# Performance work log

Measured on AMD Instinct MI355X. Metric: run time of the kernel, lower is better.

Reference implementation:

```python
import jax, jax.numpy as jnp
import numpy as np

HEIGHT = 1024.0
WIDTH = 1024.0
OUTER_BOUND_WEIGHT = 0.01


def setup_inputs() -> dict:
    key = jax.random.key(0)
    k1, k2 = jax.random.split(key)
    B, K = 4096, 4096
    # predictions roughly in-image scale
    output = jax.random.normal(k1, (B, K, 2), dtype=jnp.float32) * 300.0 + 512.0
    target = jax.random.uniform(k2, (B, K, 2), dtype=jnp.float32) * 1224.0 - 100.0
    return {"output": output, "target": target}


def reference(output, target):
    # output, target: [B, K, 2]
    B = target.shape[0]
    tx = target[..., 0]
    ty = target[..., 1]
    oob = (tx < 0) | (tx > WIDTH) | (ty < 0) | (ty > HEIGHT)  # [B, K]
    weight = jnp.where(oob, OUTER_BOUND_WEIGHT, 1.0).astype(output.dtype)
    sq = jnp.sum((output - target) ** 2, axis=-1)  # [B, K] per-keypoint MSE
    raw_batch_loss = jnp.sum(weight * sq)
    return raw_batch_loss / B
```

## Files before the change

kernel.cpp:

```cpp
#include <hip/hip_runtime.h>


#define WIDTH_F  1024.0f
#define HEIGHT_F 1024.0f
#define OOB_W    0.01f

__device__ __forceinline__ float kp_pair(float4 o, float4 t) {
    float dx = o.x - t.x;
    float dy = o.y - t.y;
    float sqA = dx * dx + dy * dy;
    bool oobA = (t.x < 0.0f) || (t.x > WIDTH_F) || (t.y < 0.0f) || (t.y > HEIGHT_F);
    float dz = o.z - t.z;
    float dw = o.w - t.w;
    float sqB = dz * dz + dw * dw;
    bool oobB = (t.z < 0.0f) || (t.z > WIDTH_F) || (t.w < 0.0f) || (t.w > HEIGHT_F);
    return (oobA ? OOB_W : 1.0f) * sqA + (oobB ? OOB_W : 1.0f) * sqB;
}

__global__ __launch_bounds__(256) void res_kp_loss_kernel(
    const float4* __restrict__ out4,
    const float4* __restrict__ tgt4,
    float* __restrict__ result,
    int n4,
    float inv_b) {
    int idx    = blockIdx.x * blockDim.x + threadIdx.x;
    int stride = gridDim.x * blockDim.x;

    float acc0 = 0.0f, acc1 = 0.0f, acc2 = 0.0f, acc3 = 0.0f;

    int i = idx;
    for (; i + 3 * stride < n4; i += 4 * stride) {
        float4 o0 = out4[i];
        float4 o1 = out4[i + stride];
        float4 o2 = out4[i + 2 * stride];
        float4 o3 = out4[i + 3 * stride];
        float4 t0 = tgt4[i];
        float4 t1 = tgt4[i + stride];
        float4 t2 = tgt4[i + 2 * stride];
        float4 t3 = tgt4[i + 3 * stride];
        acc0 += kp_pair(o0, t0);
        acc1 += kp_pair(o1, t1);
        acc2 += kp_pair(o2, t2);
        acc3 += kp_pair(o3, t3);
    }
    for (; i < n4; i += stride) {
        acc0 += kp_pair(out4[i], tgt4[i]);
    }

    float acc = (acc0 + acc1) + (acc2 + acc3);

    #pragma unroll
    for (int off = 32; off > 0; off >>= 1)
        acc += __shfl_down(acc, off, 64);

    __shared__ float wave_sums[4];
    int lane = threadIdx.x & 63;
    int wave = threadIdx.x >> 6;
    if (lane == 0) wave_sums[wave] = acc;
    __syncthreads();

    if (threadIdx.x == 0) {
        float s = (wave_sums[0] + wave_sums[1]) + (wave_sums[2] + wave_sums[3]);
        atomicAdd(result, s * inv_b);
    }
}

extern "C" void kernel_launch(void* const* d_in, const int* in_sizes, int n_in,
                              void* d_out, int out_size, void* d_ws, size_t ws_size,
                              hipStream_t stream) {
    const float4* out4 = (const float4*)d_in[0];
    const float4* tgt4 = (const float4*)d_in[1];
    float* result = (float*)d_out;

    const int total_floats = in_sizes[0];
    const int n4 = total_floats / 4;
    const float inv_b = 1.0f / 4096.0f;

    hipMemsetAsync(d_out, 0, out_size * sizeof(float), stream);

    const int block = 256;
    const int grid = 2048;
    res_kp_loss_kernel<<<grid, block, 0, stream>>>(out4, tgt4, result, n4, inv_b);
}
```

Before: 280.0 us.

## Stage input loads through LDS with direct global-to-LDS async copies

Replaces the register-based 4-way unrolled grid-stride loads with batches of 8 slots per wave that use the global_load_lds builtin to copy 16-byte elements for both inputs straight into shared memory. After a waitcnt the wave reads them back from LDS and computes the weighted squared error. The aim is more bytes in flight per wave without raising register pressure. In exchange every element takes an extra LDS round trip, and there is a full waitcnt barrier per batch with no double buffering. Using 16-byte global-to-LDS transfers also depends on support for that width on this architecture.

```diff
diff --git a/kernel.cpp b/kernel.cpp
--- a/kernel.cpp
+++ b/kernel.cpp
@@ -4,6 +4,10 @@
 #define WIDTH_F  1024.0f
 #define HEIGHT_F 1024.0f
 #define OOB_W    0.01f
+#define SLOTS    8
+
+typedef const __attribute__((address_space(1))) void* gptr_t;
+typedef __attribute__((address_space(3))) void*       lptr_t;
 
 __device__ __forceinline__ float kp_pair(float4 o, float4 t) {
     float dx = o.x - t.x;
@@ -23,43 +27,53 @@
     float* __restrict__ result,
     int n4,
     float inv_b) {
-    int idx    = blockIdx.x * blockDim.x + threadIdx.x;
-    int stride = gridDim.x * blockDim.x;
+    __shared__ float4 lds[4][SLOTS][128];
 
-    float acc0 = 0.0f, acc1 = 0.0f, acc2 = 0.0f, acc3 = 0.0f;
+    const int tid    = threadIdx.x;
+    const int wave   = tid >> 6;
+    const int lane   = tid & 63;
+    const int idx    = blockIdx.x * blockDim.x + tid;
+    const int stride = gridDim.x * blockDim.x;
 
-    int i = idx;
-    for (; i + 3 * stride < n4; i += 4 * stride) {
-        float4 o0 = out4[i];
-        float4 o1 = out4[i + stride];
-        float4 o2 = out4[i + 2 * stride];
-        float4 o3 = out4[i + 3 * stride];
-        float4 t0 = tgt4[i];
-        float4 t1 = tgt4[i + stride];
-        float4 t2 = tgt4[i + 2 * stride];
-        float4 t3 = tgt4[i + 3 * stride];
-        acc0 += kp_pair(o0, t0);
-        acc1 += kp_pair(o1, t1);
-        acc2 += kp_pair(o2, t2);
-        acc3 += kp_pair(o3, t3);
-    }
-    for (; i < n4; i += stride) {
-        acc0 += kp_pair(out4[i], tgt4[i]);
+    const int nstages = n4 / stride;
+    const int nbatch  = nstages / SLOTS;
+
+    float acc = 0.0f;
+
+    for (int b = 0; b < nbatch; ++b) {
+        const int base = b * SLOTS;
+        #pragma unroll
+        for (int s = 0; s < SLOTS; ++s) {
+            const long gi = (long)(base + s) * stride + idx;
+            __builtin_amdgcn_global_load_lds((gptr_t)(out4 + gi),
+                                             (lptr_t)&lds[wave][s][lane],
+                                             16, 0, 0);
+            __builtin_amdgcn_global_load_lds((gptr_t)(tgt4 + gi),
+                                             (lptr_t)&lds[wave][s][64 + lane],
+                                             16, 0, 0);
+        }
+        __builtin_amdgcn_s_waitcnt(0x0F70);
+        #pragma unroll
+        for (int s = 0; s < SLOTS; ++s)
+            acc += kp_pair(lds[wave][s][lane], lds[wave][s][64 + lane]);
     }
 
-    float acc = (acc0 + acc1) + (acc2 + acc3);
+    for (int s = nbatch * SLOTS; s < nstages; ++s) {
+        const long gi = (long)s * stride + idx;
+        acc += kp_pair(out4[gi], tgt4[gi]);
+    }
+    for (long i = (long)nstages * stride + idx; i < n4; i += stride)
+        acc += kp_pair(out4[i], tgt4[i]);
 
     #pragma unroll
     for (int off = 32; off > 0; off >>= 1)
         acc += __shfl_down(acc, off, 64);
 
     __shared__ float wave_sums[4];
-    int lane = threadIdx.x & 63;
-    int wave = threadIdx.x >> 6;
     if (lane == 0) wave_sums[wave] = acc;
     __syncthreads();
 
-    if (threadIdx.x == 0) {
+    if (tid == 0) {
         float s = (wave_sums[0] + wave_sums[1]) + (wave_sums[2] + wave_sums[3]);
         atomicAdd(result, s * inv_b);
     }
@@ -76,7 +90,7 @@
     const int n4 = total_floats / 4;
     const float inv_b = 1.0f / 4096.0f;
 
-    hipMemsetAsync(d_out, 0, out_size * sizeof(float), stream);
+    (void)hipMemsetAsync(d_out, 0, out_size * sizeof(float), stream);
 
     const int block = 256;
     const int grid = 2048;
```

New measurement: 279.5 us. Within noise of the previous version (-0.2%).
